# Performance work log

Hardware: AMD Instinct MI355X
Metric: run time of the kernel (lower is better)

## Reference

```python
import jax, jax.numpy as jnp
import numpy as np

N, IN_DIM, HID, OUT = 8192, 512, 256, 64
NEG_INF = -9e15


def setup_inputs() -> dict:
    key = jax.random.key(0)
    ks = jax.random.split(key, 7)
    X = jax.random.normal(ks[0], (N, IN_DIM), dtype=jnp.float32)
    A = jax.random.randint(ks[1], (N, N), 0, 2, dtype=jnp.int32)
    # fc1 (Linear): kaiming-uniform-ish init, exact dist irrelevant for correctness
    W1 = jax.random.normal(ks[2], (IN_DIM, HID), dtype=jnp.float32) / np.sqrt(IN_DIM)
    b1 = jnp.zeros((HID,), dtype=jnp.float32)
    # attention vector a: xavier_uniform(gain=1.414) on shape (2*HID, 1)
    lim = 1.414 * np.sqrt(6.0 / (2 * HID + 1))
    a = jax.random.uniform(ks[3], (2 * HID, 1), minval=-lim, maxval=lim, dtype=jnp.float32)
    Omega = jax.random.normal(ks[4], (HID, OUT), dtype=jnp.float32) * np.sqrt(2.0 / (HID + OUT))
    beta = jnp.zeros((OUT,), dtype=jnp.float32)
    return {"X": X, "A": A, "W1": W1, "b1": b1, "a": a, "Omega": Omega, "beta": beta}


def reference(X, A, W1, b1, a, Omega, beta):
    H1 = X @ W1 + b1                      # [N, HID]
    # score(i,j) = leakyrelu(a[:HID].H1_i + a[HID:].H1_j) -- computed via broadcast,
    # avoiding the O(N^2 * 2*HID) concat the torch code materializes.
    a1 = a[:HID, 0]                       # [HID]
    a2 = a[HID:, 0]                       # [HID]
    e = jax.nn.leaky_relu((H1 @ a1)[:, None] + (H1 @ a2)[None, :], negative_slope=0.2)  # [N, N]
    e = jnp.where(A > 0, e, NEG_INF)
    attention = jax.nn.softmax(e, axis=1)  # dropout_rate=0.0 -> identity
    H2 = attention @ H1                    # [N, HID]
    return jax.nn.sigmoid(H2 @ Omega + beta)  # [N, OUT]
```

## Files before the change

kernel.cpp:

```cpp
#include <hip/hip_runtime.h>
#include <hip/hip_bf16.h>


typedef float f32x4 __attribute__((ext_vector_type(4)));
typedef short s16x8 __attribute__((ext_vector_type(8)));

#define NN 8192
#define INDIM 512
#define HIDD 256
#define OUTD 64

static __device__ __forceinline__ short f2bf(float x) {
    __hip_bfloat16 h = __float2bfloat16(x);
    return __builtin_bit_cast(short, h);
}

static __device__ __forceinline__ void split_bf(float x, short& hi, short& lo) {
    short h = f2bf(x);
    unsigned int hb = ((unsigned int)(unsigned short)h) << 16;
    float hf = __builtin_bit_cast(float, hb);
    hi = h;
    lo = f2bf(x - hf);
}

__global__ void __launch_bounds__(256)
k_packA(const int* __restrict__ A, unsigned int* __restrict__ Apk) {
    const int i = blockIdx.x;
    const int t = threadIdx.x;
    const int ks = t >> 6, q = (t >> 4) & 3, kk0 = t & 15;
    const int* Ar = A + (size_t)i * NN;
    unsigned int out = 0;
#pragma unroll
    for (int kkq = 0; kkq < 4; ++kkq) {
        const int kk = kk0 * 4 + kkq;
        const int c0 = ks * 2048 + kk * 32 + q * 8;
        int4 v0 = *(const int4*)(Ar + c0);
        int4 v1 = *(const int4*)(Ar + c0 + 4);
        unsigned int b = 0;
        b |= (v0.x > 0) ? 1u : 0u;
        b |= (v0.y > 0) ? 2u : 0u;
        b |= (v0.z > 0) ? 4u : 0u;
        b |= (v0.w > 0) ? 8u : 0u;
        b |= (v1.x > 0) ? 16u : 0u;
        b |= (v1.y > 0) ? 32u : 0u;
        b |= (v1.z > 0) ? 64u : 0u;
        b |= (v1.w > 0) ? 128u : 0u;
        out |= b << (kkq * 8);
    }
    Apk[(size_t)i * 256 + t] = out;
}

__global__ void k_splitW1(const float* __restrict__ W1,
                          short* __restrict__ W1Thi, short* __restrict__ W1Tlo) {
    int t = blockIdx.x * 256 + threadIdx.x;
    int n = t >> 9;
    int k = t & 511;
    float x = W1[k * 256 + n];
    short hi, lo; split_bf(x, hi, lo);
    W1Thi[t] = hi;
    W1Tlo[t] = lo;
}

__global__ void __launch_bounds__(256, 4)
k_h1(const float* __restrict__ X, const short* __restrict__ W1Thi,
     const short* __restrict__ W1Tlo, const float* __restrict__ b1,
     const float* __restrict__ avec, unsigned short* __restrict__ H1TB,
     float* __restrict__ s1w, float* __restrict__ s2w) {
    __shared__ float s1p[4][16];
    __shared__ float s2p[4][16];
    const int tid = threadIdx.x;
    const int wn = tid >> 6, lane = tid & 63;
    const int q = lane >> 4, m16 = lane & 15;
    const int rt = blockIdx.x >> 1;
    const int ch = blockIdx.x & 1;
    const int i0 = rt * 16;
    const int irow = i0 + m16;
    const int colbase = ch * 128 + wn * 32;

    f32x4 zero4 = {0.f, 0.f, 0.f, 0.f};
    f32x4 acc[2];
#pragma unroll
    for (int nt = 0; nt < 2; ++nt) acc[nt] = zero4;

    const float* Xrow = X + (size_t)irow * INDIM;
    for (int kk = 0; kk < INDIM; kk += 32) {
        const int k0 = kk + q * 8;
        float4 xa = *(const float4*)(Xrow + k0);
        float4 xb = *(const float4*)(Xrow + k0 + 4);
        float xs[8] = {xa.x, xa.y, xa.z, xa.w, xb.x, xb.y, xb.z, xb.w};
        s16x8 ahi, alo;
#pragma unroll
        for (int j = 0; j < 8; ++j) { short h, l; split_bf(xs[j], h, l); ahi[j] = h; alo[j] = l; }
#pragma unroll
        for (int nt = 0; nt < 2; ++nt) {
            const int n = colbase + nt * 16 + m16;
            s16x8 bhi = *(const s16x8*)(W1Thi + n * INDIM + k0);
            s16x8 blo = *(const s16x8*)(W1Tlo + n * INDIM + k0);
            acc[nt] = __builtin_amdgcn_mfma_f32_16x16x32_bf16(ahi, bhi, acc[nt], 0, 0, 0);
            acc[nt] = __builtin_amdgcn_mfma_f32_16x16x32_bf16(ahi, blo, acc[nt], 0, 0, 0);
            acc[nt] = __builtin_amdgcn_mfma_f32_16x16x32_bf16(alo, bhi, acc[nt], 0, 0, 0);
        }
    }

    float p1[4] = {0.f, 0.f, 0.f, 0.f};
    float p2[4] = {0.f, 0.f, 0.f, 0.f};
    const int rowbase = i0 + q * 4;
    const int chunk = rowbase >> 5, win = rowbase & 31;
#pragma unroll
    for (int nt = 0; nt < 2; ++nt) {
        const int col = colbase + nt * 16 + m16;
        const float b1v = b1[col];
        const float a1v = avec[col];
        const float a2v = avec[HIDD + col];
        float v0 = acc[nt][0] + b1v;
        float v1 = acc[nt][1] + b1v;
        float v2 = acc[nt][2] + b1v;
        float v3 = acc[nt][3] + b1v;
        ushort4 us;
        us.x = (unsigned short)f2bf(v0);
        us.y = (unsigned short)f2bf(v1);
        us.z = (unsigned short)f2bf(v2);
        us.w = (unsigned short)f2bf(v3);
        *(ushort4*)(H1TB + (size_t)chunk * 8192 + col * 32 + win) = us;
        p1[0] += v0 * a1v; p1[1] += v1 * a1v; p1[2] += v2 * a1v; p1[3] += v3 * a1v;
        p2[0] += v0 * a2v; p2[1] += v1 * a2v; p2[2] += v2 * a2v; p2[3] += v3 * a2v;
    }
#pragma unroll
    for (int off = 1; off < 16; off <<= 1) {
#pragma unroll
        for (int r = 0; r < 4; ++r) {
            p1[r] += __shfl_xor(p1[r], off);
            p2[r] += __shfl_xor(p2[r], off);
        }
    }
    if (m16 == 0) {
#pragma unroll
        for (int r = 0; r < 4; ++r) {
            s1p[wn][q * 4 + r] = p1[r];
            s2p[wn][q * 4 + r] = p2[r];
        }
    }
    __syncthreads();
    if (tid < 16) {
        const int i = i0 + tid;
        float s1 = (s1p[0][tid] + s1p[1][tid]) + (s1p[2][tid] + s1p[3][tid]);
        float s2 = (s2p[0][tid] + s2p[1][tid]) + (s2p[2][tid] + s2p[3][tid]);
        atomicAdd(&s1w[i], s1);
        atomicAdd(&s2w[i], s2);
    }
}

__global__ void __launch_bounds__(256)
k_uv(const float* __restrict__ s1w, const float* __restrict__ s2w,
     float* __restrict__ alw, float* __restrict__ bew, float* __restrict__ uvw) {
    const int i = blockIdx.x * 256 + threadIdx.x;
    const float s1 = s1w[i], s2 = s2w[i];
    alw[i] = expf(s1);
    bew[i] = expf(0.2f * s1);
    uvw[2 * i]     = expf(s2);
    uvw[2 * i + 1] = expf(0.2f * s2);
}

__global__ void __launch_bounds__(256, 4)
k_attn(const unsigned int* __restrict__ Apk, const unsigned short* __restrict__ H1TB,
       const float* __restrict__ alw, const float* __restrict__ bew,
       const float* __restrict__ uvw,
       float* __restrict__ H2acc, float* __restrict__ Zw) {
    __shared__ unsigned short tile[2][8192];

    const int tid = threadIdx.x;
    const int wave = tid >> 6, lane = tid & 63;
    const int q = lane >> 4, m16 = lane & 15;
    const int wm = wave & 1, wn = wave >> 1;
    const int mb = blockIdx.x & 255;
    const int ks = blockIdx.x >> 8;
    const int i = mb * 32 + wm * 16 + m16;
    const float al = alw[i], be = bew[i];

    const int tswz = tid ^ ((tid >> 3) & 3);
    const unsigned short* gp = H1TB + (size_t)ks * 64 * 8192 + tswz * 8;
    __attribute__((address_space(3))) unsigned short* tl =
        (__attribute__((address_space(3))) unsigned short*)&tile[0][0];

    const unsigned int* Ab = Apk + (size_t)i * 256 + ks * 64 + q * 16;
    const float* uvp = uvw + 2 * (ks * 2048 + q * 8);

    const int hb0 = wn * 128 + m16;
    const int qx = (q * 8) ^ (((hb0 >> 1) & 3) << 3);

    f32x4 zero4 = {0.f, 0.f, 0.f, 0.f};
    f32x4 acc[8];
#pragma unroll
    for (int nt = 0; nt < 8; ++nt) acc[nt] = zero4;
    float zacc = 0.f;

#pragma unroll
    for (int c = 0; c < 4; ++c)
        __builtin_amdgcn_global_load_lds(
            (const __attribute__((address_space(1))) void*)(gp + c * 2048),
            (__attribute__((address_space(3))) void*)(tl + c * 2048 + tid * 8),
            16, 0, 0);
    gp += 8192;

    float4 uv0 = *(const float4*)(uvp);
    float4 uv1 = *(const float4*)(uvp + 4);
    float4 uv2 = *(const float4*)(uvp + 8);
    float4 uv3 = *(const float4*)(uvp + 12);
    uvp += 64;
    unsigned int a4 = Ab[0];

    for (int kk4 = 0; kk4 < 16; ++kk4) {
        unsigned int a4n = Ab[(kk4 + 1) & 15];
#pragma unroll
        for (int kkq = 0; kkq < 4; ++kkq) {
            const int kk = kk4 * 4 + kkq;
            const unsigned int ab = a4 >> (kkq * 8);

            float wv[8];
            wv[0] = (ab & 1u)   ? fmaxf(al * uv0.x, be * uv0.y) : 0.f;
            wv[1] = (ab & 2u)   ? fmaxf(al * uv0.z, be * uv0.w) : 0.f;
            wv[2] = (ab & 4u)   ? fmaxf(al * uv1.x, be * uv1.y) : 0.f;
            wv[3] = (ab & 8u)   ? fmaxf(al * uv1.z, be * uv1.w) : 0.f;
            wv[4] = (ab & 16u)  ? fmaxf(al * uv2.x, be * uv2.y) : 0.f;
            wv[5] = (ab & 32u)  ? fmaxf(al * uv2.z, be * uv2.w) : 0.f;
            wv[6] = (ab & 64u)  ? fmaxf(al * uv3.x, be * uv3.y) : 0.f;
            wv[7] = (ab & 128u) ? fmaxf(al * uv3.z, be * uv3.w) : 0.f;
            zacc += (wv[0] + wv[1] + wv[2] + wv[3]) + (wv[4] + wv[5] + wv[6] + wv[7]);
            s16x8 af;
#pragma unroll
            for (int j = 0; j < 8; ++j) af[j] = f2bf(wv[j]);

            __builtin_amdgcn_sched_barrier(0);
            if (kkq == 0) asm volatile("s_waitcnt vmcnt(1)" ::: "memory");
            else          asm volatile("s_waitcnt vmcnt(0)" ::: "memory");
            __builtin_amdgcn_s_barrier();
            __builtin_amdgcn_sched_barrier(0);

            if (kk < 63) {
                uv0 = *(const float4*)(uvp);
                uv1 = *(const float4*)(uvp + 4);
                uv2 = *(const float4*)(uvp + 8);
                uv3 = *(const float4*)(uvp + 12);
                uvp += 64;
                const int nb = ((kk + 1) & 1) * 8192;
#pragma unroll
                for (int c = 0; c < 4; ++c)
                    __builtin_amdgcn_global_load_lds(
                        (const __attribute__((address_space(1))) void*)(gp + c * 2048),
                        (__attribute__((address_space(3))) void*)(tl + nb + c * 2048 + tid * 8),
                        16, 0, 0);
                gp += 8192;
            }

            const unsigned short* tb = &tile[kk & 1][0];
#pragma unroll
            for (int nt = 0; nt < 8; ++nt) {
                s16x8 bfv = *(const s16x8*)(tb + (hb0 + nt * 16) * 32 + qx);
                acc[nt] = __builtin_amdgcn_mfma_f32_16x16x32_bf16(af, bfv, acc[nt], 0, 0, 0);
            }
        }
        a4 = a4n;
    }

    zacc += __shfl_xor(zacc, 16);
    zacc += __shfl_xor(zacc, 32);
    if (wn == 0 && q == 0) atomicAdd(&Zw[i], zacc);

    const int rowbase = mb * 32 + wm * 16 + q * 4;
#pragma unroll
    for (int nt = 0; nt < 8; ++nt) {
        const int col = wn * 128 + nt * 16 + m16;
#pragma unroll
        for (int r = 0; r < 4; ++r)
            atomicAdd(&H2acc[(size_t)(rowbase + r) * HIDD + col], acc[nt][r]);
    }
}

__global__ void __launch_bounds__(256)
k_out(const float* __restrict__ H2acc, const float* __restrict__ Zw,
      const float* __restrict__ Omega, const float* __restrict__ beta,
      float* __restrict__ out) {
    __shared__ float om[HIDD * OUTD];
    const int tid = threadIdx.x;
    for (int idx = tid; idx < HIDD * OUTD; idx += 256) om[idx] = Omega[idx];
    __syncthreads();
    const int wave = tid >> 6, o = tid & 63;
    const float bv = beta[o];
    for (int rr = 0; rr < 4; ++rr) {
        const int i = blockIdx.x * 16 + wave * 4 + rr;
        const float4* H2v = (const float4*)(H2acc + (size_t)i * HIDD);
        float acc = 0.f;
#pragma unroll 4
        for (int c4 = 0; c4 < 64; ++c4) {
            float4 h = H2v[c4];
            const int cb = c4 * 4;
            acc = fmaf(h.x, om[(cb + 0) * OUTD + o], acc);
            acc = fmaf(h.y, om[(cb + 1) * OUTD + o], acc);
            acc = fmaf(h.z, om[(cb + 2) * OUTD + o], acc);
            acc = fmaf(h.w, om[(cb + 3) * OUTD + o], acc);
        }
        const float zinv = 1.0f / Zw[i];
        const float logit = acc * zinv + bv;
        out[(size_t)i * OUTD + o] = 1.0f / (1.0f + expf(-logit));
    }
}

extern "C" void kernel_launch(void* const* d_in, const int* in_sizes, int n_in,
                              void* d_out, int out_size, void* d_ws, size_t ws_size,
                              hipStream_t stream) {
    const float* X     = (const float*)d_in[0];
    const int*   A     = (const int*)d_in[1];
    const float* W1    = (const float*)d_in[2];
    const float* b1    = (const float*)d_in[3];
    const float* avec  = (const float*)d_in[4];
    const float* Omega = (const float*)d_in[5];
    const float* beta  = (const float*)d_in[6];
    float* out = (float*)d_out;

    char* ws = (char*)d_ws;
    unsigned short* H1TB = (unsigned short*)(ws + 0);
    short* W1Thi = (short*)(ws + 4194304);
    short* W1Tlo = (short*)(ws + 4456448);
    float* s1w   = (float*)(ws + 4718592);
    float* s2w   = (float*)(ws + 4751360);
    float* alw   = (float*)(ws + 4784128);
    float* bew   = (float*)(ws + 4816896);
    float* uvw   = (float*)(ws + 4849664);
    float* Zw    = (float*)(ws + 4915200);
    float* H2acc = (float*)(ws + 4947968);
    unsigned int* Apk = (unsigned int*)(ws + 13336576);

    hipMemsetAsync(s1w, 0, 8617984, stream);

    k_splitW1<<<512, 256, 0, stream>>>(W1, W1Thi, W1Tlo);
    k_h1<<<1024, 256, 0, stream>>>(X, W1Thi, W1Tlo, b1, avec, H1TB, s1w, s2w);
    k_uv<<<32, 256, 0, stream>>>(s1w, s2w, alw, bew, uvw);
    k_packA<<<8192, 256, 0, stream>>>(A, Apk);
    k_attn<<<1024, 256, 0, stream>>>(Apk, H1TB, alw, bew, uvw, H2acc, Zw);
    k_out<<<512, 256, 0, stream>>>(H2acc, Zw, Omega, beta, out);
}
```

Baseline: 535.9 us.

## Fuse adjacency mask read into attention kernel and drop bit-packing pass

Removes the k_packA kernel that compressed the int32 adjacency matrix into bitmasks. The attention kernel now streams the raw int32 rows of A directly with nontemporal vector loads, prefetched two steps ahead in a rotating register buffer. The wait counts are adjusted so these loads stay in flight across the barrier. This avoids a full separate pass over A plus the packed-mask write and read. In exchange, the main kernel must carry the full A bandwidth itself, and the two waves sharing rows each load them, relying on cache to absorb the duplication.

```diff
diff --git a/kernel.cpp b/kernel.cpp
--- a/kernel.cpp
+++ b/kernel.cpp
@@ -4,6 +4,7 @@
 
 typedef float f32x4 __attribute__((ext_vector_type(4)));
 typedef short s16x8 __attribute__((ext_vector_type(8)));
+typedef int   i32x4 __attribute__((ext_vector_type(4)));
 
 #define NN 8192
 #define INDIM 512
@@ -21,33 +22,6 @@
     float hf = __builtin_bit_cast(float, hb);
     hi = h;
     lo = f2bf(x - hf);
-}
-
-__global__ void __launch_bounds__(256)
-k_packA(const int* __restrict__ A, unsigned int* __restrict__ Apk) {
-    const int i = blockIdx.x;
-    const int t = threadIdx.x;
-    const int ks = t >> 6, q = (t >> 4) & 3, kk0 = t & 15;
-    const int* Ar = A + (size_t)i * NN;
-    unsigned int out = 0;
-#pragma unroll
-    for (int kkq = 0; kkq < 4; ++kkq) {
-        const int kk = kk0 * 4 + kkq;
-        const int c0 = ks * 2048 + kk * 32 + q * 8;
-        int4 v0 = *(const int4*)(Ar + c0);
-        int4 v1 = *(const int4*)(Ar + c0 + 4);
-        unsigned int b = 0;
-        b |= (v0.x > 0) ? 1u : 0u;
-        b |= (v0.y > 0) ? 2u : 0u;
-        b |= (v0.z > 0) ? 4u : 0u;
-        b |= (v0.w > 0) ? 8u : 0u;
-        b |= (v1.x > 0) ? 16u : 0u;
-        b |= (v1.y > 0) ? 32u : 0u;
-        b |= (v1.z > 0) ? 64u : 0u;
-        b |= (v1.w > 0) ? 128u : 0u;
-        out |= b << (kkq * 8);
-    }
-    Apk[(size_t)i * 256 + t] = out;
 }
 
 __global__ void k_splitW1(const float* __restrict__ W1,
@@ -162,7 +136,7 @@
 }
 
 __global__ void __launch_bounds__(256, 4)
-k_attn(const unsigned int* __restrict__ Apk, const unsigned short* __restrict__ H1TB,
+k_attn(const int* __restrict__ A, const unsigned short* __restrict__ H1TB,
        const float* __restrict__ alw, const float* __restrict__ bew,
        const float* __restrict__ uvw,
        float* __restrict__ H2acc, float* __restrict__ Zw) {
@@ -182,7 +156,7 @@
     __attribute__((address_space(3))) unsigned short* tl =
         (__attribute__((address_space(3))) unsigned short*)&tile[0][0];
 
-    const unsigned int* Ab = Apk + (size_t)i * 256 + ks * 64 + q * 16;
+    const int* Arow = A + (size_t)i * NN + ks * 2048 + q * 8;
     const float* uvp = uvw + 2 * (ks * 2048 + q * 8);
 
     const int hb0 = wn * 128 + m16;
@@ -194,6 +168,16 @@
     for (int nt = 0; nt < 8; ++nt) acc[nt] = zero4;
     float zacc = 0.f;
 
+    float4 uv0 = *(const float4*)(uvp);
+    float4 uv1 = *(const float4*)(uvp + 4);
+    float4 uv2 = *(const float4*)(uvp + 8);
+    float4 uv3 = *(const float4*)(uvp + 12);
+    uvp += 64;
+    __builtin_amdgcn_sched_barrier(0);
+    i32x4 Aq0[2], Aq1[2];
+    Aq0[0] = __builtin_nontemporal_load((const i32x4*)(Arow));
+    Aq1[0] = __builtin_nontemporal_load((const i32x4*)(Arow + 4));
+    __builtin_amdgcn_sched_barrier(0);
 #pragma unroll
     for (int c = 0; c < 4; ++c)
         __builtin_amdgcn_global_load_lds(
@@ -201,38 +185,34 @@
             (__attribute__((address_space(3))) void*)(tl + c * 2048 + tid * 8),
             16, 0, 0);
     gp += 8192;
-
-    float4 uv0 = *(const float4*)(uvp);
-    float4 uv1 = *(const float4*)(uvp + 4);
-    float4 uv2 = *(const float4*)(uvp + 8);
-    float4 uv3 = *(const float4*)(uvp + 12);
-    uvp += 64;
-    unsigned int a4 = Ab[0];
+    __builtin_amdgcn_sched_barrier(0);
+    Aq0[1] = __builtin_nontemporal_load((const i32x4*)(Arow + 32));
+    Aq1[1] = __builtin_nontemporal_load((const i32x4*)(Arow + 36));
+    __builtin_amdgcn_sched_barrier(0);
 
     for (int kk4 = 0; kk4 < 16; ++kk4) {
-        unsigned int a4n = Ab[(kk4 + 1) & 15];
 #pragma unroll
         for (int kkq = 0; kkq < 4; ++kkq) {
             const int kk = kk4 * 4 + kkq;
-            const unsigned int ab = a4 >> (kkq * 8);
+            const i32x4 av0 = Aq0[kkq & 1];
+            const i32x4 av1 = Aq1[kkq & 1];
 
             float wv[8];
-            wv[0] = (ab & 1u)   ? fmaxf(al * uv0.x, be * uv0.y) : 0.f;
-            wv[1] = (ab & 2u)   ? fmaxf(al * uv0.z, be * uv0.w) : 0.f;
-            wv[2] = (ab & 4u)   ? fmaxf(al * uv1.x, be * uv1.y) : 0.f;
-            wv[3] = (ab & 8u)   ? fmaxf(al * uv1.z, be * uv1.w) : 0.f;
-            wv[4] = (ab & 16u)  ? fmaxf(al * uv2.x, be * uv2.y) : 0.f;
-            wv[5] = (ab & 32u)  ? fmaxf(al * uv2.z, be * uv2.w) : 0.f;
-            wv[6] = (ab & 64u)  ? fmaxf(al * uv3.x, be * uv3.y) : 0.f;
-            wv[7] = (ab & 128u) ? fmaxf(al * uv3.z, be * uv3.w) : 0.f;
+            wv[0] = (av0[0] > 0) ? fmaxf(al * uv0.x, be * uv0.y) : 0.f;
+            wv[1] = (av0[1] > 0) ? fmaxf(al * uv0.z, be * uv0.w) : 0.f;
+            wv[2] = (av0[2] > 0) ? fmaxf(al * uv1.x, be * uv1.y) : 0.f;
+            wv[3] = (av0[3] > 0) ? fmaxf(al * uv1.z, be * uv1.w) : 0.f;
+            wv[4] = (av1[0] > 0) ? fmaxf(al * uv2.x, be * uv2.y) : 0.f;
+            wv[5] = (av1[1] > 0) ? fmaxf(al * uv2.z, be * uv2.w) : 0.f;
+            wv[6] = (av1[2] > 0) ? fmaxf(al * uv3.x, be * uv3.y) : 0.f;
+            wv[7] = (av1[3] > 0) ? fmaxf(al * uv3.z, be * uv3.w) : 0.f;
             zacc += (wv[0] + wv[1] + wv[2] + wv[3]) + (wv[4] + wv[5] + wv[6] + wv[7]);
             s16x8 af;
 #pragma unroll
             for (int j = 0; j < 8; ++j) af[j] = f2bf(wv[j]);
 
             __builtin_amdgcn_sched_barrier(0);
-            if (kkq == 0) asm volatile("s_waitcnt vmcnt(1)" ::: "memory");
-            else          asm volatile("s_waitcnt vmcnt(0)" ::: "memory");
+            asm volatile("s_waitcnt vmcnt(2)" ::: "memory");
             __builtin_amdgcn_s_barrier();
             __builtin_amdgcn_sched_barrier(0);
 
@@ -242,6 +222,7 @@
                 uv2 = *(const float4*)(uvp + 8);
                 uv3 = *(const float4*)(uvp + 12);
                 uvp += 64;
+                __builtin_amdgcn_sched_barrier(0);
                 const int nb = ((kk + 1) & 1) * 8192;
 #pragma unroll
                 for (int c = 0; c < 4; ++c)
@@ -250,7 +231,15 @@
                         (__attribute__((address_space(3))) void*)(tl + nb + c * 2048 + tid * 8),
                         16, 0, 0);
                 gp += 8192;
+                __builtin_amdgcn_sched_barrier(0);
             }
+            {
+                const int ka = (kk + 2 <= 63) ? (kk + 2) : 63;
+                const int* ap = Arow + ka * 32;
+                Aq0[kkq & 1] = __builtin_nontemporal_load((const i32x4*)(ap));
+                Aq1[kkq & 1] = __builtin_nontemporal_load((const i32x4*)(ap + 4));
+            }
+            __builtin_amdgcn_sched_barrier(0);
 
             const unsigned short* tb = &tile[kk & 1][0];
 #pragma unroll
@@ -259,7 +248,6 @@
                 acc[nt] = __builtin_amdgcn_mfma_f32_16x16x32_bf16(af, bfv, acc[nt], 0, 0, 0);
             }
         }
-        a4 = a4n;
     }
 
     zacc += __shfl_xor(zacc, 16);
@@ -328,14 +316,12 @@
     float* uvw   = (float*)(ws + 4849664);
     float* Zw    = (float*)(ws + 4915200);
     float* H2acc = (float*)(ws + 4947968);
-    unsigned int* Apk = (unsigned int*)(ws + 13336576);
 
     hipMemsetAsync(s1w, 0, 8617984, stream);
 
     k_splitW1<<<512, 256, 0, stream>>>(W1, W1Thi, W1Tlo);
     k_h1<<<1024, 256, 0, stream>>>(X, W1Thi, W1Tlo, b1, avec, H1TB, s1w, s2w);
     k_uv<<<32, 256, 0, stream>>>(s1w, s2w, alw, bew, uvw);
-    k_packA<<<8192, 256, 0, stream>>>(A, Apk);
-    k_attn<<<1024, 256, 0, stream>>>(Apk, H1TB, alw, bew, uvw, H2acc, Zw);
+    k_attn<<<1024, 256, 0, stream>>>(A, H1TB, alw, bew, uvw, H2acc, Zw);
     k_out<<<512, 256, 0, stream>>>(H2acc, Zw, Omega, beta, out);
 }
```

Result: slower. 632.4 us (+18.0%).
